# Performance work log

Measured on AMD Instinct MI355X. Metric: run time of the kernel, lower is better.

## Reference

```python
import jax, jax.numpy as jnp
import numpy as np

SPEED_OF_SOUND = 343.0
SAMPLING_FREQUENCY = 96000.0
REC_LEN = 4096   # recording_length_samples
CROP_LEN = 128   # crop_length_samples
NUM_RECV = 8
B1, B2 = 4, 16384
HIDDEN = 32


def setup_inputs() -> dict:
    key = jax.random.key(0)
    ks = jax.random.split(key, 6)
    recordings = jax.random.normal(ks[0], (B1, NUM_RECV, REC_LEN), dtype=jnp.float32)
    sample_locations = jax.random.normal(ks[1], (B1, B2, 3), dtype=jnp.float32)
    emitter_location = jax.random.normal(ks[2], (3,), dtype=jnp.float32)
    receiver_locations = jax.random.normal(ks[3], (NUM_RECV, 3), dtype=jnp.float32)
    W1 = 0.02 * jax.random.normal(ks[4], (NUM_RECV * CROP_LEN, HIDDEN), dtype=jnp.float32)
    b1 = jnp.zeros((HIDDEN,), dtype=jnp.float32)
    W2 = 0.02 * jax.random.normal(ks[5], (HIDDEN, 1), dtype=jnp.float32)
    b2 = jnp.zeros((1,), dtype=jnp.float32)
    return {
        "recordings": recordings,
        "sample_locations": sample_locations,
        "emitter_location": emitter_location,
        "receiver_locations": receiver_locations,
        "W1": W1, "b1": b1, "W2": W2, "b2": b2,
    }


def reference(recordings, sample_locations, emitter_location, receiver_locations, W1, b1, W2, b2):
    # recordings: (B1, R, L); sample_locations: (B1, B2, 3)
    b1_, R, L = recordings.shape
    b2_ = sample_locations.shape[1]
    K = W1.shape[0] // R  # crop_length_samples

    # time-of-flight distances
    d_emit = jnp.linalg.norm(sample_locations - emitter_location, axis=-1)              # (B1, B2)
    d_recv = jnp.linalg.norm(sample_locations[:, :, None, :] - receiver_locations, axis=-1)  # (B1, B2, R)
    total_samples = jnp.round((d_emit[..., None] + d_recv) / SPEED_OF_SOUND * SAMPLING_FREQUENCY)
    crop_start = total_samples - K // 2                                                  # (B1, B2, R)

    # normalized grid coordinates, exactly as in the torch module
    grid_base = -1.0 + 2.0 * (crop_start / L)                                            # (B1, B2, R)
    grid_offset = jnp.linspace(0.0, 0.5 * (K - 1) / L, K, dtype=jnp.float32)             # (K,)
    gx = grid_base[..., None] + grid_offset                                              # (B1, B2, R, K)

    # Exact torch grid_sample(mode='bilinear', align_corners=False, zero padding) on
    # input of shape (N, 1, H=L, W=1) with grid = (x=gx, y=0). In torch, x indexes the
    # WIDTH dim (size 1) and y=0 indexes the HEIGHT dim (size L), so:
    #   iy = ((0+1)*L - 1)/2 = (L-1)/2  (constant -> blend of the two center samples)
    #   ix = ((gx+1)*1 - 1)/2 = gx/2    (triangle weight around the single width pixel)
    iy = (L - 1) / 2.0
    iy0 = int(np.floor(iy))
    wy1 = jnp.float32(iy - iy0)
    wy0 = jnp.float32(1.0) - wy1
    vy = wy0 * recordings[..., iy0] + wy1 * recordings[..., iy0 + 1]                     # (B1, R)

    ix = gx * 0.5
    ix0 = jnp.floor(ix)
    fx = ix - ix0
    # corner at width index ix0 is in-bounds iff ix0 == 0; corner ix0+1 iff ix0 == -1
    w = (1.0 - fx) * (ix0 == 0.0).astype(ix.dtype) + fx * (ix0 == -1.0).astype(ix.dtype)
    crops = w * vy[:, None, :, None]                                                     # (B1, B2, R, K)

    # tiny MLP head
    x = crops.reshape(b1_ * b2_, R * K)
    h = jax.nn.relu(x @ W1 + b1)
    pred = (h @ W2 + b2).reshape(b1_, b2_)
    return pred
```

## Files before the change

### kernel.cpp

```cpp
#include <hip/hip_runtime.h>
#include <math.h>

#define PQ_STRIDE (129 * 256)

__global__ __launch_bounds__(256) void prep(const float* __restrict__ W1,
                                            float* __restrict__ P,
                                            float* __restrict__ Q) {
  __shared__ float slab[2 * 128 * 32];
  const int t = threadIdx.x;
  const int r0 = blockIdx.x * 2;
  const float4* src = (const float4*)(W1 + r0 * 128 * 32);
  float4* dst = (float4*)slab;
#pragma unroll
  for (int i = 0; i < 8; i++) dst[t + i * 256] = src[t + i * 256];
  __syncthreads();
  if (t < 64) {
    const int rl = t >> 5, h = t & 31;
    const int r = r0 + rl;
    float p = 0.f, q = 0.f;
    for (int k = 0; k < 128; k++) {
      P[k * 256 + r * 32 + h] = p;
      Q[k * 256 + r * 32 + h] = q;
      const float w = slab[(rl * 128 + k) * 32 + h];
      p += w;
      q = fmaf((float)k * (1.0f / 16384.0f), w, q);
    }
    P[128 * 256 + r * 32 + h] = p;
    Q[128 * 256 + r * 32 + h] = q;
  }
}

__global__ __launch_bounds__(256) void tof_main(
    const float* __restrict__ recordings, const float* __restrict__ sloc,
    const float* __restrict__ emit, const float* __restrict__ rloc,
    const float* __restrict__ b1v, const float* __restrict__ W2,
    const float* __restrict__ b2v, const float* __restrict__ Pg,
    const float* __restrict__ Qg, float* __restrict__ out) {
  __shared__ __align__(16) float Ps[256];
  __shared__ __align__(16) float Qs[256];
  __shared__ __align__(16) float b1s[32];
  __shared__ __align__(16) float W2s[32];
  __shared__ float vys[8];
  __shared__ float ems[3];
  __shared__ float rls[24];
  __shared__ float b2s;
  const int t = threadIdx.x;
  const int sid = blockIdx.x * 256 + t;
  const int b = sid >> 14;

  if (t < 64) {
    ((float4*)Ps)[t] = ((const float4*)(Pg + 128 * 256))[t];
  } else if (t < 128) {
    ((float4*)Qs)[t - 64] = ((const float4*)(Qg + 128 * 256))[t - 64];
  } else if (t < 152) {
    rls[t - 128] = rloc[t - 128];
  } else if (t < 155) {
    ems[t - 152] = emit[t - 152];
  } else if (t == 155) {
    b2s = b2v[0];
  } else if (t >= 160 && t < 168) {
    const int r = t - 160;
    const float* rp = recordings + ((b << 3) + r) * 4096;
    vys[r] = 0.5f * (rp[2047] + rp[2048]);
  } else if (t >= 192 && t < 224) {
    b1s[t - 192] = b1v[t - 192];
  } else if (t >= 224) {
    W2s[t - 224] = W2[t - 224];
  }
  __syncthreads();

  const float xx = sloc[3 * sid + 0];
  const float yy = sloc[3 * sid + 1];
  const float zz = sloc[3 * sid + 2];
  const float ex = xx - ems[0], ey = yy - ems[1], ez = zz - ems[2];
  const float de = sqrtf(ex * ex + ey * ey + ez * ez);

  float4 acc[8];
#pragma unroll
  for (int q = 0; q < 8; q++) acc[q] = make_float4(0.f, 0.f, 0.f, 0.f);

#pragma unroll
  for (int r = 0; r < 8; r++) {
    const float rx = xx - rls[3 * r + 0];
    const float ry = yy - rls[3 * r + 1];
    const float rz = zz - rls[3 * r + 2];
    const float dr = sqrtf(rx * rx + ry * ry + rz * rz);
    const float ts = rintf(((de + dr) / 343.0f) * 96000.0f);
    const int T = (int)ts;
    const float g0 = (ts - 64.0f) * (1.0f / 2048.0f) - 1.0f;
    const float vr = vys[r];
    const bool fast1 = (T <= 2080);
    const bool fast3 = (T >= 2112) && (T <= 6176);
    if (fast1 | fast3) {
      const float sg = fast1 ? 1.0f : -1.0f;
      const float aa = vr * fmaf(0.5f * sg, g0, 1.0f);
      const float cc = sg * vr;
      const float4* Pr = (const float4*)(Ps + r * 32);
      const float4* Qr = (const float4*)(Qs + r * 32);
#pragma unroll
      for (int q = 0; q < 8; q++) {
        const float4 pv = Pr[q];
        const float4 qv = Qr[q];
        acc[q].x = fmaf(aa, pv.x, fmaf(cc, qv.x, acc[q].x));
        acc[q].y = fmaf(aa, pv.y, fmaf(cc, qv.y, acc[q].y));
        acc[q].z = fmaf(aa, pv.z, fmaf(cc, qv.z, acc[q].z));
        acc[q].w = fmaf(aa, pv.w, fmaf(cc, qv.w, acc[q].w));
      }
    } else {
      int ka = 8448 - 4 * T;  ka = min(max(ka, 0), 128);
      int kb = 24832 - 4 * T; kb = min(max(kb, 0), 128);
      const float u = fmaf(0.5f, g0, 1.0f);
      const float v = fmaf(-0.5f, g0, 1.0f);
      const float4* Pa = (const float4*)(Pg + ka * 256 + r * 32);
      const float4* Qa = (const float4*)(Qg + ka * 256 + r * 32);
      const float4* Pb = (const float4*)(Pg + kb * 256 + r * 32);
      const float4* Qb = (const float4*)(Qg + kb * 256 + r * 32);
#pragma unroll
      for (int q = 0; q < 8; q++) {
        const float4 pa = Pa[q], qa = Qa[q], pb = Pb[q], qb = Qb[q];
        const float s0 = u * pa.x + qa.x + v * (pb.x - pa.x) - (qb.x - qa.x);
        const float s1 = u * pa.y + qa.y + v * (pb.y - pa.y) - (qb.y - qa.y);
        const float s2 = u * pa.z + qa.z + v * (pb.z - pa.z) - (qb.z - qa.z);
        const float s3 = u * pa.w + qa.w + v * (pb.w - pa.w) - (qb.w - qa.w);
        acc[q].x = fmaf(vr, s0, acc[q].x);
        acc[q].y = fmaf(vr, s1, acc[q].y);
        acc[q].z = fmaf(vr, s2, acc[q].z);
        acc[q].w = fmaf(vr, s3, acc[q].w);
      }
    }
  }

  float pred = b2s;
  const float4* b14 = (const float4*)b1s;
  const float4* W24 = (const float4*)W2s;
#pragma unroll
  for (int q = 0; q < 8; q++) {
    const float4 hb = b14[q];
    const float4 wv = W24[q];
    pred = fmaf(fmaxf(acc[q].x + hb.x, 0.0f), wv.x, pred);
    pred = fmaf(fmaxf(acc[q].y + hb.y, 0.0f), wv.y, pred);
    pred = fmaf(fmaxf(acc[q].z + hb.z, 0.0f), wv.z, pred);
    pred = fmaf(fmaxf(acc[q].w + hb.w, 0.0f), wv.w, pred);
  }
  out[sid] = pred;
}

__global__ __launch_bounds__(256) void tof_fused(
    const float* __restrict__ recordings, const float* __restrict__ sloc,
    const float* __restrict__ emit, const float* __restrict__ rloc,
    const float* __restrict__ W1, const float* __restrict__ b1v,
    const float* __restrict__ W2, const float* __restrict__ b2v,
    float* __restrict__ out) {
  __shared__ float vy[8];
  __shared__ float em[3];
  __shared__ float rl[24];
  __shared__ float b1s[32];
  __shared__ float W2s[32];
  __shared__ float b2s;
  const int t = threadIdx.x;
  const int sid = blockIdx.x * 256 + t;
  const int b = sid >> 14;

  if (t < 8) {
    const float* rp = recordings + ((b << 3) + t) * 4096;
    vy[t] = 0.5f * (rp[2047] + rp[2048]);
  }
  if (t < 3) em[t] = emit[t];
  if (t >= 32 && t < 56) rl[t - 32] = rloc[t - 32];
  if (t >= 64 && t < 96) b1s[t - 64] = b1v[t - 64];
  if (t >= 96 && t < 128) W2s[t - 96] = W2[t - 96];
  if (t == 128) b2s = b2v[0];
  __syncthreads();

  const float x = sloc[sid * 3 + 0];
  const float y = sloc[sid * 3 + 1];
  const float z = sloc[sid * 3 + 2];
  const float ex = x - em[0], ey = y - em[1], ez = z - em[2];
  const float de = sqrtf(ex * ex + ey * ey + ez * ez);

  float acc[32];
#pragma unroll
  for (int h = 0; h < 32; h++) acc[h] = 0.f;

  for (int r = 0; r < 8; r++) {
    const float rx = x - rl[r * 3 + 0];
    const float ry = y - rl[r * 3 + 1];
    const float rz = z - rl[r * 3 + 2];
    const float dr = sqrtf(rx * rx + ry * ry + rz * rz);
    const float ts = rintf(((de + dr) / 343.0f) * 96000.0f);
    const float g0 = ts * (1.0f / 2048.0f) - (1.0f + 64.0f / 2048.0f);
    const float vr = vy[r];
    for (int k = 0; k < 128; k++) {
      const float gx = g0 + (float)k * (1.0f / 8192.0f);
      const float w = fmaxf(0.0f, fmaf(-0.5f, fabsf(gx), 1.0f));
      const float c = w * vr;
      const float* wrow = W1 + (((r << 7) + k) << 5);
#pragma unroll
      for (int h = 0; h < 32; h++) acc[h] = fmaf(c, wrow[h], acc[h]);
    }
  }

  float pred = b2s;
#pragma unroll
  for (int h = 0; h < 32; h++) {
    const float hv = fmaxf(acc[h] + b1s[h], 0.0f);
    pred = fmaf(hv, W2s[h], pred);
  }
  out[sid] = pred;
}

extern "C" void kernel_launch(void* const* d_in, const int* in_sizes, int n_in,
                              void* d_out, int out_size, void* d_ws,
                              size_t ws_size, hipStream_t stream) {
  const float* recordings = (const float*)d_in[0];
  const float* sloc       = (const float*)d_in[1];
  const float* emit       = (const float*)d_in[2];
  const float* rloc       = (const float*)d_in[3];
  const float* W1         = (const float*)d_in[4];
  const float* b1v        = (const float*)d_in[5];
  const float* W2         = (const float*)d_in[6];
  const float* b2v        = (const float*)d_in[7];
  float* out = (float*)d_out;

  const size_t pq_bytes = (size_t)2 * PQ_STRIDE * sizeof(float);
  if (ws_size >= pq_bytes) {
    float* P = (float*)d_ws;
    float* Q = P + PQ_STRIDE;
    prep<<<4, 256, 0, stream>>>(W1, P, Q);
    tof_main<<<256, 256, 0, stream>>>(recordings, sloc, emit, rloc, b1v, W2,
                                      b2v, P, Q, out);
  } else {
    tof_fused<<<256, 256, 0, stream>>>(recordings, sloc, emit, rloc, W1, b1v,
                                       W2, b2v, out);
  }
}
```

Before: 82.99 us.

## Fuse W1 prefix-sum prep into main kernel and drop workspace tables

Removes the separate prep kernel and the full prefix-sum P/Q tables. Each block now computes only the total column sums of W1 per receiver/hidden unit into shared memory, and the rare partial-overlap case falls back to a direct 128-step loop over W1. This saves a kernel launch and the serialized prep work, in exchange for every block redundantly reading all of W1 (128 KB) and a slower path for edge-case samples.

```diff
diff --git a/kernel.cpp b/kernel.cpp
--- a/kernel.cpp
+++ b/kernel.cpp
@@ -1,41 +1,12 @@
 #include <hip/hip_runtime.h>
 #include <math.h>
 
-#define PQ_STRIDE (129 * 256)
-
-__global__ __launch_bounds__(256) void prep(const float* __restrict__ W1,
-                                            float* __restrict__ P,
-                                            float* __restrict__ Q) {
-  __shared__ float slab[2 * 128 * 32];
-  const int t = threadIdx.x;
-  const int r0 = blockIdx.x * 2;
-  const float4* src = (const float4*)(W1 + r0 * 128 * 32);
-  float4* dst = (float4*)slab;
-#pragma unroll
-  for (int i = 0; i < 8; i++) dst[t + i * 256] = src[t + i * 256];
-  __syncthreads();
-  if (t < 64) {
-    const int rl = t >> 5, h = t & 31;
-    const int r = r0 + rl;
-    float p = 0.f, q = 0.f;
-    for (int k = 0; k < 128; k++) {
-      P[k * 256 + r * 32 + h] = p;
-      Q[k * 256 + r * 32 + h] = q;
-      const float w = slab[(rl * 128 + k) * 32 + h];
-      p += w;
-      q = fmaf((float)k * (1.0f / 16384.0f), w, q);
-    }
-    P[128 * 256 + r * 32 + h] = p;
-    Q[128 * 256 + r * 32 + h] = q;
-  }
-}
-
-__global__ __launch_bounds__(256) void tof_main(
+__global__ __launch_bounds__(256) void tof_all(
     const float* __restrict__ recordings, const float* __restrict__ sloc,
     const float* __restrict__ emit, const float* __restrict__ rloc,
-    const float* __restrict__ b1v, const float* __restrict__ W2,
-    const float* __restrict__ b2v, const float* __restrict__ Pg,
-    const float* __restrict__ Qg, float* __restrict__ out) {
+    const float* __restrict__ W1, const float* __restrict__ b1v,
+    const float* __restrict__ W2, const float* __restrict__ b2v,
+    float* __restrict__ out) {
   __shared__ __align__(16) float Ps[256];
   __shared__ __align__(16) float Qs[256];
   __shared__ __align__(16) float b1s[32];
@@ -44,28 +15,39 @@
   __shared__ float ems[3];
   __shared__ float rls[24];
   __shared__ float b2s;
+
   const int t = threadIdx.x;
   const int sid = blockIdx.x * 256 + t;
   const int b = sid >> 14;
 
-  if (t < 64) {
-    ((float4*)Ps)[t] = ((const float4*)(Pg + 128 * 256))[t];
-  } else if (t < 128) {
-    ((float4*)Qs)[t - 64] = ((const float4*)(Qg + 128 * 256))[t - 64];
-  } else if (t < 152) {
-    rls[t - 128] = rloc[t - 128];
-  } else if (t < 155) {
-    ems[t - 152] = emit[t - 152];
-  } else if (t == 155) {
+  if (t < 24) {
+    rls[t] = rloc[t];
+  } else if (t < 27) {
+    ems[t - 24] = emit[t - 24];
+  } else if (t == 27) {
     b2s = b2v[0];
-  } else if (t >= 160 && t < 168) {
-    const int r = t - 160;
+  } else if (t >= 32 && t < 40) {
+    const int r = t - 32;
     const float* rp = recordings + ((b << 3) + r) * 4096;
     vys[r] = 0.5f * (rp[2047] + rp[2048]);
-  } else if (t >= 192 && t < 224) {
-    b1s[t - 192] = b1v[t - 192];
-  } else if (t >= 224) {
-    W2s[t - 224] = W2[t - 224];
+  } else if (t >= 64 && t < 96) {
+    b1s[t - 64] = b1v[t - 64];
+  } else if (t >= 96 && t < 128) {
+    W2s[t - 96] = W2[t - 96];
+  }
+
+  {
+    const int r = t >> 5, h = t & 31;
+    const float* wp = W1 + (r << 12) + h;
+    float p = 0.f, q = 0.f;
+#pragma unroll 8
+    for (int k = 0; k < 128; k++) {
+      const float w = wp[k << 5];
+      p += w;
+      q = fmaf((float)k * (1.0f / 16384.0f), w, q);
+    }
+    Ps[t] = p;
+    Qs[t] = q;
   }
   __syncthreads();
 
@@ -107,25 +89,20 @@
         acc[q].w = fmaf(aa, pv.w, fmaf(cc, qv.w, acc[q].w));
       }
     } else {
-      int ka = 8448 - 4 * T;  ka = min(max(ka, 0), 128);
-      int kb = 24832 - 4 * T; kb = min(max(kb, 0), 128);
-      const float u = fmaf(0.5f, g0, 1.0f);
-      const float v = fmaf(-0.5f, g0, 1.0f);
-      const float4* Pa = (const float4*)(Pg + ka * 256 + r * 32);
-      const float4* Qa = (const float4*)(Qg + ka * 256 + r * 32);
-      const float4* Pb = (const float4*)(Pg + kb * 256 + r * 32);
-      const float4* Qb = (const float4*)(Qg + kb * 256 + r * 32);
+#pragma unroll 1
+      for (int k = 0; k < 128; k++) {
+        const float gx = fmaf((float)k, (1.0f / 8192.0f), g0);
+        const float w = fmaxf(0.0f, fmaf(-0.5f, fabsf(gx), 1.0f));
+        const float c = w * vr;
+        const float4* w4 = (const float4*)(W1 + (((r << 7) + k) << 5));
 #pragma unroll
-      for (int q = 0; q < 8; q++) {
-        const float4 pa = Pa[q], qa = Qa[q], pb = Pb[q], qb = Qb[q];
-        const float s0 = u * pa.x + qa.x + v * (pb.x - pa.x) - (qb.x - qa.x);
-        const float s1 = u * pa.y + qa.y + v * (pb.y - pa.y) - (qb.y - qa.y);
-        const float s2 = u * pa.z + qa.z + v * (pb.z - pa.z) - (qb.z - qa.z);
-        const float s3 = u * pa.w + qa.w + v * (pb.w - pa.w) - (qb.w - qa.w);
-        acc[q].x = fmaf(vr, s0, acc[q].x);
-        acc[q].y = fmaf(vr, s1, acc[q].y);
-        acc[q].z = fmaf(vr, s2, acc[q].z);
-        acc[q].w = fmaf(vr, s3, acc[q].w);
+        for (int q = 0; q < 8; q++) {
+          const float4 wv = w4[q];
+          acc[q].x = fmaf(c, wv.x, acc[q].x);
+          acc[q].y = fmaf(c, wv.y, acc[q].y);
+          acc[q].z = fmaf(c, wv.z, acc[q].z);
+          acc[q].w = fmaf(c, wv.w, acc[q].w);
+        }
       }
     }
   }
@@ -145,70 +122,6 @@
   out[sid] = pred;
 }
 
-__global__ __launch_bounds__(256) void tof_fused(
-    const float* __restrict__ recordings, const float* __restrict__ sloc,
-    const float* __restrict__ emit, const float* __restrict__ rloc,
-    const float* __restrict__ W1, const float* __restrict__ b1v,
-    const float* __restrict__ W2, const float* __restrict__ b2v,
-    float* __restrict__ out) {
-  __shared__ float vy[8];
-  __shared__ float em[3];
-  __shared__ float rl[24];
-  __shared__ float b1s[32];
-  __shared__ float W2s[32];
-  __shared__ float b2s;
-  const int t = threadIdx.x;
-  const int sid = blockIdx.x * 256 + t;
-  const int b = sid >> 14;
-
-  if (t < 8) {
-    const float* rp = recordings + ((b << 3) + t) * 4096;
-    vy[t] = 0.5f * (rp[2047] + rp[2048]);
-  }
-  if (t < 3) em[t] = emit[t];
-  if (t >= 32 && t < 56) rl[t - 32] = rloc[t - 32];
-  if (t >= 64 && t < 96) b1s[t - 64] = b1v[t - 64];
-  if (t >= 96 && t < 128) W2s[t - 96] = W2[t - 96];
-  if (t == 128) b2s = b2v[0];
-  __syncthreads();
-
-  const float x = sloc[sid * 3 + 0];
-  const float y = sloc[sid * 3 + 1];
-  const float z = sloc[sid * 3 + 2];
-  const float ex = x - em[0], ey = y - em[1], ez = z - em[2];
-  const float de = sqrtf(ex * ex + ey * ey + ez * ez);
-
-  float acc[32];
-#pragma unroll
-  for (int h = 0; h < 32; h++) acc[h] = 0.f;
-
-  for (int r = 0; r < 8; r++) {
-    const float rx = x - rl[r * 3 + 0];
-    const float ry = y - rl[r * 3 + 1];
-    const float rz = z - rl[r * 3 + 2];
-    const float dr = sqrtf(rx * rx + ry * ry + rz * rz);
-    const float ts = rintf(((de + dr) / 343.0f) * 96000.0f);
-    const float g0 = ts * (1.0f / 2048.0f) - (1.0f + 64.0f / 2048.0f);
-    const float vr = vy[r];
-    for (int k = 0; k < 128; k++) {
-      const float gx = g0 + (float)k * (1.0f / 8192.0f);
-      const float w = fmaxf(0.0f, fmaf(-0.5f, fabsf(gx), 1.0f));
-      const float c = w * vr;
-      const float* wrow = W1 + (((r << 7) + k) << 5);
-#pragma unroll
-      for (int h = 0; h < 32; h++) acc[h] = fmaf(c, wrow[h], acc[h]);
-    }
-  }
-
-  float pred = b2s;
-#pragma unroll
-  for (int h = 0; h < 32; h++) {
-    const float hv = fmaxf(acc[h] + b1s[h], 0.0f);
-    pred = fmaf(hv, W2s[h], pred);
-  }
-  out[sid] = pred;
-}
-
 extern "C" void kernel_launch(void* const* d_in, const int* in_sizes, int n_in,
                               void* d_out, int out_size, void* d_ws,
                               size_t ws_size, hipStream_t stream) {
@@ -222,15 +135,8 @@
   const float* b2v        = (const float*)d_in[7];
   float* out = (float*)d_out;
 
-  const size_t pq_bytes = (size_t)2 * PQ_STRIDE * sizeof(float);
-  if (ws_size >= pq_bytes) {
-    float* P = (float*)d_ws;
-    float* Q = P + PQ_STRIDE;
-    prep<<<4, 256, 0, stream>>>(W1, P, Q);
-    tof_main<<<256, 256, 0, stream>>>(recordings, sloc, emit, rloc, b1v, W2,
-                                      b2v, P, Q, out);
-  } else {
-    tof_fused<<<256, 256, 0, stream>>>(recordings, sloc, emit, rloc, W1, b1v,
-                                       W2, b2v, out);
-  }
+  (void)d_ws; (void)ws_size;
+
+  tof_all<<<256, 256, 0, stream>>>(recordings, sloc, emit, rloc, W1, b1v, W2,
+                                   b2v, out);
 }
```

Result: slower. 194.2 us (+134.0%).
